# Kernel tuning notes

Hardware: AMD Instinct MI355X
Metric: run time of the kernel (lower is better)

Reference implementation:

```python
import jax, jax.numpy as jnp
import numpy as np

HIDDEN = 2048
N_HEADS = 16
HEAD_DIM = HIDDEN // N_HEADS
ROPE_THETA = 10000.0
BSZ, SEQ = 2, 2048
NEG_INF = -1e9


def setup_inputs() -> dict:
    key = jax.random.key(0)
    ks = jax.random.split(key, 5)
    scale = 1.0 / np.sqrt(HIDDEN)
    hidden_states = jax.random.normal(ks[0], (BSZ, SEQ, HIDDEN), dtype=jnp.float32)
    Wq = jax.random.normal(ks[1], (HIDDEN, HIDDEN), dtype=jnp.float32) * scale
    Wk = jax.random.normal(ks[2], (HIDDEN, HIDDEN), dtype=jnp.float32) * scale
    Wv = jax.random.normal(ks[3], (HIDDEN, HIDDEN), dtype=jnp.float32) * scale
    Wo = jax.random.normal(ks[4], (HIDDEN, HIDDEN), dtype=jnp.float32) * scale
    # additive causal mask, [1, 1, S, S]
    causal = jnp.triu(jnp.full((SEQ, SEQ), NEG_INF, dtype=jnp.float32), k=1)
    attention_mask = causal[None, None, :, :]
    position_ids = jnp.arange(SEQ, dtype=jnp.int32)
    return {
        "hidden_states": hidden_states,
        "Wq": Wq, "Wk": Wk, "Wv": Wv, "Wo": Wo,
        "attention_mask": attention_mask,
        "position_ids": position_ids,
    }


def _rotate_half(x):
    half = x.shape[-1] // 2
    return jnp.concatenate((-x[..., half:], x[..., :half]), axis=-1)


def _rope_tables(seq_len, position_ids):
    # inv_freq: [head_dim/2]
    inv_freq = 1.0 / (ROPE_THETA ** (jnp.arange(0, HEAD_DIM, 2, dtype=jnp.float32) / HEAD_DIM))
    t = jnp.arange(seq_len, dtype=jnp.float32)
    freqs = t[:, None] * inv_freq[None, :]              # [S, D/2]
    emb = jnp.concatenate((freqs, freqs), axis=-1)      # [S, D]
    cos = jnp.cos(emb)[position_ids]                    # [S, D]
    sin = jnp.sin(emb)[position_ids]
    return cos, sin


def reference(hidden_states, Wq, Wk, Wv, Wo, attention_mask, position_ids):
    b, s, h = hidden_states.shape
    def proj(W):
        return (hidden_states @ W.T).reshape(b, s, N_HEADS, HEAD_DIM).transpose(0, 2, 1, 3)
    q = proj(Wq)  # [B, H, S, D]
    k = proj(Wk)
    v = proj(Wv)
    cos, sin = _rope_tables(s, position_ids)            # [S, D], broadcasts over B,H
    q = q * cos + _rotate_half(q) * sin
    k = k * cos + _rotate_half(k) * sin
    scores = jnp.einsum('bhqd,bhkd->bhqk', q, k) / np.sqrt(HEAD_DIM)
    scores = scores + attention_mask
    w = jax.nn.softmax(scores, axis=-1)
    out = jnp.einsum('bhqk,bhkd->bhqd', w, v)           # [B, H, S, D]
    out = out.transpose(0, 2, 1, 3).reshape(b, s, h)
    return out @ Wo.T
```

## Files before the change

kernel.cpp:

```cpp
#include <hip/hip_runtime.h>
#include <cstdint>
#include <cstddef>

typedef __bf16 bf16;
typedef __bf16 bf16x4 __attribute__((ext_vector_type(4)));
typedef __bf16 bf16x8 __attribute__((ext_vector_type(8)));
typedef float  f32x4  __attribute__((ext_vector_type(4)));
typedef short  s16x4  __attribute__((ext_vector_type(4)));

#define HIDDEN 2048
#define NHEADS 16
#define HDIM   128
#define BSZ    2
#define SEQ    2048
#define BS     (BSZ*SEQ)
#define QKW    (2*HIDDEN)

union b4u { bf16x4 h; s16x4 s; };

__device__ __forceinline__ void async16(const bf16* g, bf16* l) {
    __builtin_amdgcn_global_load_lds(
        (const __attribute__((address_space(1))) unsigned int*)g,
        (__attribute__((address_space(3))) unsigned int*)l, 16, 0, 0);
}

#define BARX()  asm volatile("s_barrier" ::: "memory")
#define VMW(N)  asm volatile("s_waitcnt vmcnt(" #N ")" ::: "memory")

__global__ __launch_bounds__(256) void cast_all(const float* __restrict__ hs,
                                                const float* __restrict__ Wq,
                                                const float* __restrict__ Wk,
                                                const float* __restrict__ Wv,
                                                const float* __restrict__ Wo,
                                                const int* __restrict__ pos,
                                                bf16* __restrict__ hs_b,
                                                bf16* __restrict__ wqkv,
                                                bf16* __restrict__ wo_b,
                                                float2* __restrict__ tab) {
    int i = blockIdx.x * 256 + threadIdx.x;
    if (i >= 6291456) {
        int j = i - 6291456;
        int s = j >> 6, p = j & 63;
        float t = (float)pos[s];
        float inv = expf(-(float)(2 * p) * (9.2103403719761836f / 128.0f));
        float sn, cs;
        sincosf(t * inv, &sn, &cs);
        tab[j] = make_float2(cs, sn);
        return;
    }
    const float* src; bf16* dst; int off;
    if (i < 2097152) { src = hs; dst = hs_b; off = i; }
    else {
        int j = i - 2097152;
        int r = j >> 20;
        off = j & 1048575;
        if      (r == 0) { src = Wq; dst = wqkv; }
        else if (r == 1) { src = Wk; dst = wqkv + (size_t)4194304; }
        else if (r == 2) { src = Wv; dst = wqkv + (size_t)8388608; }
        else             { src = Wo; dst = wo_b; }
    }
    const float4 v = ((const float4*)src)[off];
    bf16x4 o;
    o.x = (bf16)v.x; o.y = (bf16)v.y; o.z = (bf16)v.z; o.w = (bf16)v.w;
    ((bf16x4*)dst)[off] = o;
}

__device__ __forceinline__ int qk_perm(int n) {
    int wl = n >> 6, j = n & 63;
    return ((wl >> 1) << 7) | ((j >> 5) << 6) | ((wl & 1) << 5) | (j & 31);
}

#define QKV_TILE(T, DOSTAGE, VMN) do {                                          \
    VMW(VMN);                                                                   \
    BARX();                                                                     \
    const bf16* lAr = lA0 + ((T) & 3) * 16384;                                  \
    const bf16* lBr = lB0 + ((T) & 3) * 16384;                                  \
    bf16x8 bfr[4], af[4];                                                       \
    _Pragma("unroll") for (int nf = 0; nf < 4; ++nf)                            \
        bfr[nf] = *(const bf16x8*)(lBr + nf * 512);                             \
    _Pragma("unroll") for (int mf = 0; mf < 4; ++mf)                            \
        af[mf] = *(const bf16x8*)(lAr + mf * 512);                              \
    if (DOSTAGE) {                                                              \
        bf16* dA = smem + (((T) + 3) & 3) * 16384 + w * 512;                    \
        async16(pa0 + ((T) + 3) * 32, dA);                                      \
        async16(pa1 + ((T) + 3) * 32, dA + 4096);                               \
    }                                                                           \
    __builtin_amdgcn_s_setprio(1);                                              \
    _Pragma("unroll") for (int mf = 0; mf < 4; ++mf)                            \
    _Pragma("unroll") for (int nf = 0; nf < 4; ++nf)                            \
        acc[mf][nf] = __builtin_amdgcn_mfma_f32_16x16x32_bf16(                  \
            af[mf], bfr[nf], acc[mf][nf], 0, 0, 0);                             \
    __builtin_amdgcn_s_setprio(0);                                              \
    _Pragma("unroll") for (int mf = 0; mf < 4; ++mf)                            \
        af[mf] = *(const bf16x8*)(lAr + 2048 + mf * 512);                       \
    if (DOSTAGE) {                                                              \
        bf16* dB = smem + (((T) + 3) & 3) * 16384 + 8192 + w * 512;             \
        async16(pb0 + ((T) + 3) * 32, dB);                                      \
        async16(pb1 + ((T) + 3) * 32, dB + 4096);                               \
    }                                                                           \
    __builtin_amdgcn_s_setprio(1);                                              \
    _Pragma("unroll") for (int mf = 0; mf < 4; ++mf)                            \
    _Pragma("unroll") for (int nf = 0; nf < 4; ++nf)                            \
        acc[4 + mf][nf] = __builtin_amdgcn_mfma_f32_16x16x32_bf16(              \
            af[mf], bfr[nf], acc[4 + mf][nf], 0, 0, 0);                         \
    __builtin_amdgcn_s_setprio(0);                                              \
} while (0)

__global__ __launch_bounds__(512, 2) void gemm_qk(const bf16* __restrict__ A,
                                                  const bf16* __restrict__ Bt,
                                                  const float2* __restrict__ tab,
                                                  bf16* __restrict__ qk) {
    __shared__ alignas(16) bf16 smem[65536];

    const int tid  = threadIdx.x;
    const int lane = tid & 63;
    const int w    = tid >> 6;
    const int l15  = lane & 15;
    const int quad = lane >> 4;
    const int wm   = w >> 2;
    const int wn   = w & 3;

    const int raw = blockIdx.x;
    const int kq  = raw >> 3;
    const int mTile = (kq & 15) * 256;
    const int nTile = (2 * (raw & 7) + (kq >> 4)) * 256;

    const int sRow  = w * 16 + (lane >> 2);
    const int sColE = ((lane & 3) * 8) ^ ((lane & 32) ? 16 : 0);
    const bf16* pa0 = A + (size_t)(mTile + sRow) * HIDDEN + sColE;
    const bf16* pa1 = pa0 + (size_t)128 * HIDDEN;
    const int n0 = qk_perm(sRow), n1 = qk_perm(sRow + 128);
    const bf16* pb0 = Bt + (size_t)(nTile + n0) * HIDDEN + sColE;
    const bf16* pb1 = Bt + (size_t)(nTile + n1) * HIDDEN + sColE;

    const int colE = (quad * 8) ^ ((l15 & 8) ? 16 : 0);
    const bf16* lA0 = smem + (wm * 128 + l15) * 32 + colE;
    const bf16* lB0 = smem + 8192 + (wn * 64 + l15) * 32 + colE;

    f32x4 acc[8][4];
#pragma unroll
    for (int i = 0; i < 8; ++i)
#pragma unroll
        for (int j = 0; j < 4; ++j) acc[i][j] = (f32x4){0.f, 0.f, 0.f, 0.f};

#pragma unroll
    for (int tt = 0; tt < 3; ++tt) {
        bf16* dA = smem + tt * 16384 + w * 512;
        async16(pa0 + tt * 32, dA);
        async16(pa1 + tt * 32, dA + 4096);
        async16(pb0 + tt * 32, dA + 8192);
        async16(pb1 + tt * 32, dA + 12288);
    }

#pragma unroll 4
    for (int t = 0; t < 60; ++t) QKV_TILE(t, 1, 8);
    QKV_TILE(60, 1, 8);
    QKV_TILE(61, 0, 8);
    QKV_TILE(62, 0, 4);
    QKV_TILE(63, 0, 0);

    const int hbase = nTile + (wn >> 1) * 128 + (wn & 1) * 32;
#pragma unroll
    for (int mf = 0; mf < 8; ++mf)
#pragma unroll
        for (int r = 0; r < 4; ++r) {
            int row = mTile + wm * 128 + mf * 16 + quad * 4 + r;
            int s   = row & (SEQ - 1);
            float2 t0 = tab[s * 64 + (wn & 1) * 32 + l15];
            float2 t1 = tab[s * 64 + (wn & 1) * 32 + 16 + l15];
            size_t rb = (size_t)row * QKW + hbase + l15;
            float lo0 = acc[mf][0][r], hi0 = acc[mf][2][r];
            float lo1 = acc[mf][1][r], hi1 = acc[mf][3][r];
            qk[rb]      = (bf16)(lo0 * t0.x - hi0 * t0.y);
            qk[rb + 64] = (bf16)(hi0 * t0.x + lo0 * t0.y);
            qk[rb + 16] = (bf16)(lo1 * t1.x - hi1 * t1.y);
            qk[rb + 80] = (bf16)(hi1 * t1.x + lo1 * t1.y);
        }
}

#define OUT_TILE(T, DOSTAGE, VMN) do {                                          \
    VMW(VMN);                                                                   \
    BARX();                                                                     \
    const bf16* lAr = lA0 + ((T) & 3) * 12288;                                  \
    const bf16* lBr = lB0 + ((T) & 3) * 12288;                                  \
    bf16x8 bfr[4], af[4];                                                       \
    _Pragma("unroll") for (int nf = 0; nf < 4; ++nf)                            \
        bfr[nf] = *(const bf16x8*)(lBr + nf * 512);                             \
    _Pragma("unroll") for (int mf = 0; mf < 4; ++mf)                            \
        af[mf] = *(const bf16x8*)(lAr + mf * 512);                              \
    if (DOSTAGE) {                                                              \
        bf16* dS = smem + (((T) + 3) & 3) * 12288 + w * 512;                    \
        async16(pa0 + ((T) + 3) * 32, dS);                                      \
        async16(pb0 + ((T) + 3) * 32, dS + 4096);                               \
        async16(pb1 + ((T) + 3) * 32, dS + 8192);                               \
    }                                                                           \
    __builtin_amdgcn_s_setprio(1);                                              \
    _Pragma("unroll") for (int mf = 0; mf < 4; ++mf)                            \
    _Pragma("unroll") for (int nf = 0; nf < 4; ++nf)                            \
        acc[mf][nf] = __builtin_amdgcn_mfma_f32_16x16x32_bf16(                  \
            af[mf], bfr[nf], acc[mf][nf], 0, 0, 0);                             \
    __builtin_amdgcn_s_setprio(0);                                              \
} while (0)

#define OUT_PROLOGUE()                                                          \
    const int tid  = threadIdx.x;                                               \
    const int lane = tid & 63;                                                  \
    const int w    = tid >> 6;                                                  \
    const int l15  = lane & 15;                                                 \
    const int quad = lane >> 4;                                                 \
    const int wm   = w >> 2;                                                    \
    const int wn   = w & 3;                                                     \
    const int raw = blockIdx.x;                                                 \
    const int mTile = (raw >> 3) * 128;                                         \
    const int nTile = (raw & 7) * 256;                                          \
    const int sRow  = w * 16 + (lane >> 2);                                     \
    const int sColE = ((lane & 3) * 8) ^ ((lane & 32) ? 16 : 0);                \
    const bf16* pa0 = A + (size_t)(mTile + sRow) * HIDDEN + sColE;              \
    const bf16* pb0 = Bt + (size_t)(nTile + sRow) * HIDDEN + sColE;             \
    const bf16* pb1 = pb0 + (size_t)128 * HIDDEN;                               \
    const int colE = (quad * 8) ^ ((l15 & 8) ? 16 : 0);                         \
    const bf16* lA0 = smem + (wm * 64 + l15) * 32 + colE;                       \
    const bf16* lB0 = smem + 4096 + (wn * 64 + l15) * 32 + colE;                \
    f32x4 acc[4][4];                                                            \
    _Pragma("unroll") for (int i = 0; i < 4; ++i)                               \
    _Pragma("unroll") for (int j = 0; j < 4; ++j)                               \
        acc[i][j] = (f32x4){0.f, 0.f, 0.f, 0.f};                                \
    _Pragma("unroll") for (int tt = 0; tt < 3; ++tt) {                          \
        bf16* dS = smem + tt * 12288 + w * 512;                                 \
        async16(pa0 + tt * 32, dS);                                             \
        async16(pb0 + tt * 32, dS + 4096);                                      \
        async16(pb1 + tt * 32, dS + 8192);                                      \
    }                                                                           \
    _Pragma("unroll 4") for (int t = 0; t < 60; ++t) OUT_TILE(t, 1, 6);         \
    OUT_TILE(60, 1, 6);                                                         \
    OUT_TILE(61, 0, 6);                                                         \
    OUT_TILE(62, 0, 3);                                                         \
    OUT_TILE(63, 0, 0);

__global__ __launch_bounds__(512, 2) void gemm_v(const bf16* __restrict__ A,
                                                 const bf16* __restrict__ Bt,
                                                 bf16* __restrict__ vtb) {
    __shared__ alignas(16) bf16 smem[49152];
    OUT_PROLOGUE()
#pragma unroll
    for (int mf = 0; mf < 4; ++mf)
#pragma unroll
        for (int nf = 0; nf < 4; ++nf) {
            int col_v = nTile + wn * 64 + nf * 16 + l15;
            int row0  = mTile + wm * 64 + mf * 16 + quad * 4;
            bf16x4 pk;
#pragma unroll
            for (int r = 0; r < 4; ++r) pk[r] = (bf16)acc[mf][nf][r];
            *(bf16x4*)(vtb + (size_t)col_v * BS + row0) = pk;
        }
}

__global__ __launch_bounds__(512, 2) void gemm_out(const bf16* __restrict__ A,
                                                   const bf16* __restrict__ Bt,
                                                   float* __restrict__ C) {
    __shared__ alignas(16) bf16 smem[49152];
    OUT_PROLOGUE()
#pragma unroll
    for (int mf = 0; mf < 4; ++mf)
#pragma unroll
        for (int nf = 0; nf < 4; ++nf)
#pragma unroll
            for (int r = 0; r < 4; ++r) {
                int row = mTile + wm * 64 + mf * 16 + quad * 4 + r;
                int col = nTile + wn * 64 + nf * 16 + l15;
                C[(size_t)row * HIDDEN + col] = acc[mf][nf][r];
            }
}

__global__ __launch_bounds__(256) void attn_kernel(const bf16* __restrict__ qk,
                                                   const bf16* __restrict__ vt,
                                                   bf16* __restrict__ ao) {
    __shared__ bf16 Kls[2][64 * 128];
    __shared__ bf16 Vls[2][128 * 64];

    const int tid  = threadIdx.x;
    const int lane = tid & 63;
    const int w    = tid >> 6;
    const int l15  = lane & 15;
    const int quad = lane >> 4;
    const int bid  = blockIdx.x;
    const int qt   = 31 - (bid >> 5);
    const int bh   = bid & 31;
    const int b    = bh >> 4;
    const int h    = bh & 15;
    const int qbase = qt * 64;
    const size_t seq0 = (size_t)b * SEQ;

    bf16x8 qf[4];
    {
        const bf16* qp = qk + (seq0 + qbase + w * 16 + l15) * QKW + h * HDIM + quad * 8;
#pragma unroll
        for (int ks = 0; ks < 4; ++ks) qf[ks] = *(const bf16x8*)(qp + ks * 32);
    }
#pragma unroll
    for (int ks = 0; ks < 4; ++ks)
        asm volatile("" :: "v"(*(const f32x4*)&qf[ks]));

    f32x4 o[8];
#pragma unroll
    for (int i = 0; i < 8; ++i) o[i] = (f32x4){0.f, 0.f, 0.f, 0.f};
    float m_s = -3e38f, l_s = 0.f;
    const int qg = qbase + w * 16 + l15;

    const int krow = lane >> 4;
    const int kp   = lane & 15;
    const int vrow = lane >> 3;
    const int vp   = lane & 7;
    const int sw   = l15 & 7;

#define ATTN_STAGE(T, BUF) do {                                                  \
        const int kb_ = (T) * 64;                                                \
        _Pragma("unroll") for (int i = 0; i < 4; ++i) {                          \
            int j = w * 16 + i * 4 + krow;                                       \
            int c = (kp & 8) | ((kp & 7) ^ (j & 7));                             \
            async16(qk + (seq0 + kb_ + j) * QKW + HIDDEN + h * HDIM + c * 8,     \
                    &Kls[BUF][(w * 4 + i) * 512]);                               \
        }                                                                        \
        _Pragma("unroll") for (int i = 0; i < 4; ++i) {                          \
            int d = w * 32 + i * 8 + vrow;                                       \
            int c = vp ^ (d & 7);                                                \
            async16(vt + (size_t)(h * HDIM + d) * (size_t)BS + seq0 + kb_ + c * 8,\
                    &Vls[BUF][(w * 4 + i) * 512]);                               \
        }                                                                        \
    } while (0)

    ATTN_STAGE(0, 0);

    for (int t = 0; t <= qt; ++t) {
        if (t < qt) { ATTN_STAGE(t + 1, (t + 1) & 1); VMW(8); }
        else        { VMW(0); }
        BARX();
        const bf16* Kb = Kls[t & 1];
        const bf16* Vb = Vls[t & 1];
        const int kb = t * 64;

        f32x4 sa[4];
#pragma unroll
        for (int ni = 0; ni < 4; ++ni) sa[ni] = (f32x4){0.f, 0.f, 0.f, 0.f};
#pragma unroll
        for (int ni = 0; ni < 4; ++ni)
#pragma unroll
            for (int ks = 0; ks < 4; ++ks) {
                bf16x8 kf = *(const bf16x8*)(Kb + (ni * 16 + l15) * 128 +
                                             (((ks * 4 + quad) ^ sw) << 3));
                sa[ni] = __builtin_amdgcn_mfma_f32_16x16x32_bf16(kf, qf[ks], sa[ni], 0, 0, 0);
            }

        const float scale = 0.08838834764831845f * 1.4426950408889634f;
        float rmax = -3e38f;
        const bool diag = (t == qt);
#pragma unroll
        for (int ni = 0; ni < 4; ++ni)
#pragma unroll
            for (int r = 0; r < 4; ++r) {
                float sv = sa[ni][r] * scale;
                if (diag) {
                    int jg = kb + ni * 16 + quad * 4 + r;
                    if (jg > qg) sv = -1e30f;
                }
                sa[ni][r] = sv;
                rmax = fmaxf(rmax, sv);
            }
        rmax = fmaxf(rmax, __shfl_xor(rmax, 16));
        rmax = fmaxf(rmax, __shfl_xor(rmax, 32));

        float mn = fmaxf(m_s, rmax);
        float alpha = exp2f(m_s - mn);
        m_s = mn;
        float rsum = 0.f;
        b4u pb[4];
#pragma unroll
        for (int ni = 0; ni < 4; ++ni)
#pragma unroll
            for (int r = 0; r < 4; ++r) {
                float e = exp2f(sa[ni][r] - mn);
                rsum += e;
                pb[ni].h[r] = (bf16)e;
            }
        rsum += __shfl_xor(rsum, 16);
        rsum += __shfl_xor(rsum, 32);
        l_s = l_s * alpha + rsum;

        if (__ballot(alpha != 1.f) != 0ull) {
#pragma unroll
            for (int n2 = 0; n2 < 8; ++n2)
#pragma unroll
                for (int r = 0; r < 4; ++r) o[n2][r] *= alpha;
        }

#pragma unroll
        for (int n2 = 0; n2 < 8; ++n2)
#pragma unroll
            for (int ni = 0; ni < 4; ++ni) {
                b4u vf;
                vf.h = *(const bf16x4*)(Vb + (n2 * 16 + l15) * 64 +
                                        ((((ni * 2 + (quad >> 1)) ^ sw) << 3) + (quad & 1) * 4));
                o[n2] = __builtin_amdgcn_mfma_f32_16x16x16bf16_1k(vf.s, pb[ni].s, o[n2], 0, 0, 0);
            }
        BARX();
    }
#undef ATTN_STAGE

    const float inv = 1.0f / l_s;
    bf16* op = ao + (seq0 + qg) * HIDDEN + h * HDIM + quad * 4;
#pragma unroll
    for (int n2 = 0; n2 < 8; ++n2) {
        bf16x4 pk;
#pragma unroll
        for (int r = 0; r < 4; ++r) pk[r] = (bf16)(o[n2][r] * inv);
        *(bf16x4*)(op + n2 * 16) = pk;
    }
}

extern "C" void kernel_launch(void* const* d_in, const int* in_sizes, int n_in,
                              void* d_out, int out_size, void* d_ws, size_t ws_size,
                              hipStream_t stream) {
    const float* hs = (const float*)d_in[0];
    const float* Wq = (const float*)d_in[1];
    const float* Wk = (const float*)d_in[2];
    const float* Wv = (const float*)d_in[3];
    const float* Wo = (const float*)d_in[4];
    const int* pos  = (const int*)d_in[6];
    float* out = (float*)d_out;

    bf16* hs_b = (bf16*)d_ws;
    bf16* wqkv = hs_b + (size_t)8388608;
    bf16* wo_b = wqkv + (size_t)12582912;
    bf16* qkb  = wo_b + (size_t)4194304;
    bf16* vtb  = qkb + (size_t)16777216;
    bf16* ao   = vtb + (size_t)8388608;
    float2* tab = (float2*)ao;

    cast_all<<<25088, 256, 0, stream>>>(hs, Wq, Wk, Wv, Wo, pos, hs_b, wqkv, wo_b, tab);
    gemm_qk<<<256, 512, 0, stream>>>(hs_b, wqkv, tab, qkb);
    gemm_v<<<256, 512, 0, stream>>>(hs_b, wqkv + (size_t)8388608, vtb);
    attn_kernel<<<1024, 256, 0, stream>>>(qkb, vtb, ao);
    gemm_out<<<256, 512, 0, stream>>>(ao, wo_b, out);
}
```

Measured before the change: 361.8 us.

## Use 128-row query blocks with 8 waves and fold softmax scale into Q

The attention kernel now runs 512-thread blocks covering 128 query rows, so each K/V tile staged in shared memory serves twice as many queries. Blocks are launched as heavy/light query-block pairs to balance the causal workload. The softmax scale and log2(e) factor move into the Q epilogue of the QK projection GEMM, and exp2 is replaced by raw v_exp_f32. Rescaling of the running max is skipped unless it grows by more than 8, and load address offsets are precomputed. Lazy rescaling and raw exp slightly change numerics, and the larger blocks reduce how many blocks are resident at once.

```diff
diff --git a/kernel.cpp b/kernel.cpp
--- a/kernel.cpp
+++ b/kernel.cpp
@@ -26,6 +26,10 @@
 
 #define BARX()  asm volatile("s_barrier" ::: "memory")
 #define VMW(N)  asm volatile("s_waitcnt vmcnt(" #N ")" ::: "memory")
+
+__device__ __forceinline__ float ex2(float x) {
+    float r; asm("v_exp_f32 %0, %1" : "=v"(r) : "v"(x)); return r;
+}
 
 __global__ __launch_bounds__(256) void cast_all(const float* __restrict__ hs,
                                                 const float* __restrict__ Wq,
@@ -159,6 +163,7 @@
     QKV_TILE(62, 0, 4);
     QKV_TILE(63, 0, 0);
 
+    const float qs = (nTile < HIDDEN) ? (0.08838834764831845f * 1.4426950408889634f) : 1.0f;
     const int hbase = nTile + (wn >> 1) * 128 + (wn & 1) * 32;
 #pragma unroll
     for (int mf = 0; mf < 8; ++mf)
@@ -171,10 +176,10 @@
             size_t rb = (size_t)row * QKW + hbase + l15;
             float lo0 = acc[mf][0][r], hi0 = acc[mf][2][r];
             float lo1 = acc[mf][1][r], hi1 = acc[mf][3][r];
-            qk[rb]      = (bf16)(lo0 * t0.x - hi0 * t0.y);
-            qk[rb + 64] = (bf16)(hi0 * t0.x + lo0 * t0.y);
-            qk[rb + 16] = (bf16)(lo1 * t1.x - hi1 * t1.y);
-            qk[rb + 80] = (bf16)(hi1 * t1.x + lo1 * t1.y);
+            qk[rb]      = (bf16)((lo0 * t0.x - hi0 * t0.y) * qs);
+            qk[rb + 64] = (bf16)((hi0 * t0.x + lo0 * t0.y) * qs);
+            qk[rb + 16] = (bf16)((lo1 * t1.x - hi1 * t1.y) * qs);
+            qk[rb + 80] = (bf16)((hi1 * t1.x + lo1 * t1.y) * qs);
         }
 }
 
@@ -272,9 +277,9 @@
             }
 }
 
-__global__ __launch_bounds__(256) void attn_kernel(const bf16* __restrict__ qk,
-                                                   const bf16* __restrict__ vt,
-                                                   bf16* __restrict__ ao) {
+__global__ __launch_bounds__(512, 4) void attn_kernel(const bf16* __restrict__ qk,
+                                                      const bf16* __restrict__ vt,
+                                                      bf16* __restrict__ ao) {
     __shared__ bf16 Kls[2][64 * 128];
     __shared__ bf16 Vls[2][128 * 64];
 
@@ -284,11 +289,14 @@
     const int l15  = lane & 15;
     const int quad = lane >> 4;
     const int bid  = blockIdx.x;
-    const int qt   = 31 - (bid >> 5);
-    const int bh   = bid & 31;
+    const int half = bid >> 8;
+    const int idx  = bid & 255;
+    const int qb2  = half ? (idx >> 5) : 15 - (idx >> 5);
+    const int bh   = idx & 31;
     const int b    = bh >> 4;
     const int h    = bh & 15;
-    const int qbase = qt * 64;
+    const int qbase = qb2 * 128;
+    const int nt    = 2 * qb2 + 2;
     const size_t seq0 = (size_t)b * SEQ;
 
     bf16x8 qf[4];
@@ -313,97 +321,96 @@
     const int vp   = lane & 7;
     const int sw   = l15 & 7;
 
+    const bf16* qksrc = qk + seq0 * QKW + HIDDEN + h * HDIM;
+    const bf16* vtsrc = vt + (size_t)h * HDIM * BS + seq0;
+    int koff[2], voff[2];
+#pragma unroll
+    for (int i = 0; i < 2; ++i) {
+        int c = w * 2 + i;
+        int j = c * 4 + krow;
+        int c2 = (kp & 8) | ((kp & 7) ^ (j & 7));
+        koff[i] = j * QKW + c2 * 8;
+        int d = c * 8 + vrow;
+        int cv = vp ^ (d & 7);
+        voff[i] = d * BS + cv * 8;
+    }
+
+    const bf16* kbase[4];
+#pragma unroll
+    for (int ks = 0; ks < 4; ++ks)
+        kbase[ks] = &Kls[0][l15 * 128 + (((ks * 4 + quad) ^ sw) << 3)];
+    const bf16* vbase[4];
+#pragma unroll
+    for (int ni = 0; ni < 4; ++ni)
+        vbase[ni] = &Vls[0][l15 * 64 + ((((ni * 2 + (quad >> 1)) ^ sw) << 3) + (quad & 1) * 4)];
+
 #define ATTN_STAGE(T, BUF) do {                                                  \
         const int kb_ = (T) * 64;                                                \
-        _Pragma("unroll") for (int i = 0; i < 4; ++i) {                          \
-            int j = w * 16 + i * 4 + krow;                                       \
-            int c = (kp & 8) | ((kp & 7) ^ (j & 7));                             \
-            async16(qk + (seq0 + kb_ + j) * QKW + HIDDEN + h * HDIM + c * 8,     \
-                    &Kls[BUF][(w * 4 + i) * 512]);                               \
+        _Pragma("unroll") for (int i = 0; i < 2; ++i)                            \
+            async16(qksrc + (size_t)kb_ * QKW + koff[i],                         \
+                    &Kls[BUF][(w * 2 + i) * 512]);                               \
+        _Pragma("unroll") for (int i = 0; i < 2; ++i)                            \
+            async16(vtsrc + kb_ + voff[i],                                       \
+                    &Vls[BUF][(w * 2 + i) * 512]);                               \
+    } while (0)
+
+#define ATTN_TILE(T, BUF) do {                                                   \
+        if ((T) + 1 < nt) { ATTN_STAGE((T) + 1, (BUF) ^ 1); VMW(4); }            \
+        else              { VMW(0); }                                            \
+        BARX();                                                                  \
+        const int kb = (T) * 64;                                                 \
+        f32x4 sa[4];                                                             \
+        _Pragma("unroll") for (int ni = 0; ni < 4; ++ni)                         \
+            sa[ni] = (f32x4){0.f, 0.f, 0.f, 0.f};                                \
+        _Pragma("unroll") for (int ni = 0; ni < 4; ++ni)                         \
+        _Pragma("unroll") for (int ks = 0; ks < 4; ++ks) {                       \
+            bf16x8 kf = *(const bf16x8*)(kbase[ks] + (BUF) * 8192 + ni * 2048);  \
+            sa[ni] = __builtin_amdgcn_mfma_f32_16x16x32_bf16(kf, qf[ks], sa[ni], 0, 0, 0); \
         }                                                                        \
-        _Pragma("unroll") for (int i = 0; i < 4; ++i) {                          \
-            int d = w * 32 + i * 8 + vrow;                                       \
-            int c = vp ^ (d & 7);                                                \
-            async16(vt + (size_t)(h * HDIM + d) * (size_t)BS + seq0 + kb_ + c * 8,\
-                    &Vls[BUF][(w * 4 + i) * 512]);                               \
+        float rmax = -3e38f;                                                     \
+        const bool diag = ((T) >= nt - 2);                                       \
+        _Pragma("unroll") for (int ni = 0; ni < 4; ++ni)                         \
+        _Pragma("unroll") for (int r = 0; r < 4; ++r) {                          \
+            float sv = sa[ni][r];                                                \
+            if (diag && (kb + ni * 16 + quad * 4 + r > qg)) sv = -1e30f;         \
+            sa[ni][r] = sv;                                                      \
+            rmax = fmaxf(rmax, sv);                                              \
         }                                                                        \
+        rmax = fmaxf(rmax, __shfl_xor(rmax, 16));                                \
+        rmax = fmaxf(rmax, __shfl_xor(rmax, 32));                                \
+        if (__ballot(rmax > m_s + 8.f) != 0ull) {                                \
+            float mn = fmaxf(m_s, rmax);                                         \
+            float al = ex2(m_s - mn);                                            \
+            m_s = mn; l_s *= al;                                                 \
+            _Pragma("unroll") for (int n2 = 0; n2 < 8; ++n2)                     \
+            _Pragma("unroll") for (int r = 0; r < 4; ++r) o[n2][r] *= al;        \
+        }                                                                        \
+        float rsum = 0.f;                                                        \
+        b4u pb[4];                                                               \
+        _Pragma("unroll") for (int ni = 0; ni < 4; ++ni)                         \
+        _Pragma("unroll") for (int r = 0; r < 4; ++r) {                          \
+            float e = ex2(sa[ni][r] - m_s);                                      \
+            rsum += e;                                                           \
+            pb[ni].h[r] = (bf16)e;                                               \
+        }                                                                        \
+        rsum += __shfl_xor(rsum, 16);                                            \
+        rsum += __shfl_xor(rsum, 32);                                            \
+        l_s += rsum;                                                             \
+        _Pragma("unroll") for (int n2 = 0; n2 < 8; ++n2)                         \
+        _Pragma("unroll") for (int ni = 0; ni < 4; ++ni) {                       \
+            b4u vf;                                                              \
+            vf.h = *(const bf16x4*)(vbase[ni] + (BUF) * 8192 + n2 * 1024);       \
+            o[n2] = __builtin_amdgcn_mfma_f32_16x16x16bf16_1k(vf.s, pb[ni].s, o[n2], 0, 0, 0); \
+        }                                                                        \
+        BARX();                                                                  \
     } while (0)
 
     ATTN_STAGE(0, 0);
-
-    for (int t = 0; t <= qt; ++t) {
-        if (t < qt) { ATTN_STAGE(t + 1, (t + 1) & 1); VMW(8); }
-        else        { VMW(0); }
-        BARX();
-        const bf16* Kb = Kls[t & 1];
-        const bf16* Vb = Vls[t & 1];
-        const int kb = t * 64;
-
-        f32x4 sa[4];
-#pragma unroll
-        for (int ni = 0; ni < 4; ++ni) sa[ni] = (f32x4){0.f, 0.f, 0.f, 0.f};
-#pragma unroll
-        for (int ni = 0; ni < 4; ++ni)
-#pragma unroll
-            for (int ks = 0; ks < 4; ++ks) {
-                bf16x8 kf = *(const bf16x8*)(Kb + (ni * 16 + l15) * 128 +
-                                             (((ks * 4 + quad) ^ sw) << 3));
-                sa[ni] = __builtin_amdgcn_mfma_f32_16x16x32_bf16(kf, qf[ks], sa[ni], 0, 0, 0);
-            }
-
-        const float scale = 0.08838834764831845f * 1.4426950408889634f;
-        float rmax = -3e38f;
-        const bool diag = (t == qt);
-#pragma unroll
-        for (int ni = 0; ni < 4; ++ni)
-#pragma unroll
-            for (int r = 0; r < 4; ++r) {
-                float sv = sa[ni][r] * scale;
-                if (diag) {
-                    int jg = kb + ni * 16 + quad * 4 + r;
-                    if (jg > qg) sv = -1e30f;
-                }
-                sa[ni][r] = sv;
-                rmax = fmaxf(rmax, sv);
-            }
-        rmax = fmaxf(rmax, __shfl_xor(rmax, 16));
-        rmax = fmaxf(rmax, __shfl_xor(rmax, 32));
-
-        float mn = fmaxf(m_s, rmax);
-        float alpha = exp2f(m_s - mn);
-        m_s = mn;
-        float rsum = 0.f;
-        b4u pb[4];
-#pragma unroll
-        for (int ni = 0; ni < 4; ++ni)
-#pragma unroll
-            for (int r = 0; r < 4; ++r) {
-                float e = exp2f(sa[ni][r] - mn);
-                rsum += e;
-                pb[ni].h[r] = (bf16)e;
-            }
-        rsum += __shfl_xor(rsum, 16);
-        rsum += __shfl_xor(rsum, 32);
-        l_s = l_s * alpha + rsum;
-
-        if (__ballot(alpha != 1.f) != 0ull) {
-#pragma unroll
-            for (int n2 = 0; n2 < 8; ++n2)
-#pragma unroll
-                for (int r = 0; r < 4; ++r) o[n2][r] *= alpha;
-        }
-
-#pragma unroll
-        for (int n2 = 0; n2 < 8; ++n2)
-#pragma unroll
-            for (int ni = 0; ni < 4; ++ni) {
-                b4u vf;
-                vf.h = *(const bf16x4*)(Vb + (n2 * 16 + l15) * 64 +
-                                        ((((ni * 2 + (quad >> 1)) ^ sw) << 3) + (quad & 1) * 4));
-                o[n2] = __builtin_amdgcn_mfma_f32_16x16x16bf16_1k(vf.s, pb[ni].s, o[n2], 0, 0, 0);
-            }
-        BARX();
-    }
+    for (int t = 0; t < nt; t += 2) {
+        ATTN_TILE(t, 0);
+        ATTN_TILE(t + 1, 1);
+    }
+#undef ATTN_TILE
 #undef ATTN_STAGE
 
     const float inv = 1.0f / l_s;
@@ -439,6 +446,6 @@
     cast_all<<<25088, 256, 0, stream>>>(hs, Wq, Wk, Wv, Wo, pos, hs_b, wqkv, wo_b, tab);
     gemm_qk<<<256, 512, 0, stream>>>(hs_b, wqkv, tab, qkb);
     gemm_v<<<256, 512, 0, stream>>>(hs_b, wqkv + (size_t)8388608, vtb);
-    attn_kernel<<<1024, 256, 0, stream>>>(qkb, vtb, ao);
+    attn_kernel<<<512, 512, 0, stream>>>(qkb, vtb, ao);
     gemm_out<<<256, 512, 0, stream>>>(ao, wo_b, out);
 }
```

Measured after the change: 359.4 us (median of 3 runs). About the same (-0.7%).
